# Kernel optimization log

Measured on AMD Instinct MI355X. Metric: run time of the kernel, lower is better.

The kernel has to match this reference:

```python
import jax, jax.numpy as jnp
import numpy as np

D_MODEL = 1024
D_T = 256
N_HEADS = 16
HIDDEN = 4 * D_MODEL
EPS = 1e-6


def setup_inputs() -> dict:
    key = jax.random.key(0)
    ks = jax.random.split(key, 20)
    B, L = 8, 1024
    s_d = 1.0 / np.sqrt(D_MODEL)
    s_t = 1.0 / np.sqrt(D_T)
    s_h = 1.0 / np.sqrt(HIDDEN)
    return {
        "x": jax.random.normal(ks[0], (B, L, D_MODEL), jnp.float32),
        "t": jax.random.normal(ks[1], (B, D_T), jnp.float32),
        "Wq": jax.random.normal(ks[2], (D_MODEL, D_MODEL), jnp.float32) * s_d,
        "Wk": jax.random.normal(ks[3], (D_MODEL, D_MODEL), jnp.float32) * s_d,
        "Wv": jax.random.normal(ks[4], (D_MODEL, D_MODEL), jnp.float32) * s_d,
        "Wo": jax.random.normal(ks[5], (D_MODEL, D_MODEL), jnp.float32) * s_d,
        "g1w": jax.random.normal(ks[6], (D_MODEL, D_T), jnp.float32) * s_t,
        "g1b": jnp.ones((D_MODEL,), jnp.float32),
        "b1w": jax.random.normal(ks[7], (D_MODEL, D_T), jnp.float32) * s_t,
        "b1b": jnp.zeros((D_MODEL,), jnp.float32),
        "g2w": jax.random.normal(ks[8], (D_MODEL, D_T), jnp.float32) * s_t,
        "g2b": jnp.ones((D_MODEL,), jnp.float32),
        "b2w": jax.random.normal(ks[9], (D_MODEL, D_T), jnp.float32) * s_t,
        "b2b": jnp.zeros((D_MODEL,), jnp.float32),
        "gate_w": jax.random.normal(ks[10], (HIDDEN, D_MODEL), jnp.float32) * s_d,
        "hid_w": jax.random.normal(ks[11], (HIDDEN, D_MODEL), jnp.float32) * s_d,
        "out_w": jax.random.normal(ks[12], (D_MODEL, HIDDEN), jnp.float32) * s_h,
    }


def _tc_rmsnorm(x, t, gw, gb, bw, bb):
    # gamma/beta: [B, d_model] from linear on t, broadcast over L
    g = (t @ gw.T + gb)[:, None, :]
    b = (t @ bw.T + bb)[:, None, :]
    inv_rms = jax.lax.rsqrt(jnp.mean(x * x, axis=-1, keepdims=True) + EPS)
    return g * x * inv_rms + b


def _attention(x, Wq, Wk, Wv, Wo):
    B, L, D = x.shape
    H = N_HEADS
    dh = D // H
    scale = np.sqrt(dh).astype(np.float32)
    q = (x @ Wq.T).reshape(B, L, H, dh)
    k = (x @ Wk.T).reshape(B, L, H, dh)
    v = (x @ Wv.T).reshape(B, L, H, dh)
    attn = jnp.einsum("blhd,bmhd->bhlm", q, k) / scale
    p = jax.nn.softmax(attn, axis=-1)
    o = jnp.einsum("bhlm,bmhd->blhd", p, v).reshape(B, L, D)
    return o @ Wo.T


def _swiglu(x, gate_w, hid_w, out_w):
    return (jax.nn.silu(x @ gate_w.T) * (x @ hid_w.T)) @ out_w.T


def reference(x, t, Wq, Wk, Wv, Wo, g1w, g1b, b1w, b1b, g2w, g2b, b2w, b2b, gate_w, hid_w, out_w):
    x = x + _attention(_tc_rmsnorm(x, t, g1w, g1b, b1w, b1b), Wq, Wk, Wv, Wo)
    return x + _swiglu(_tc_rmsnorm(x, t, g2w, g2b, b2w, b2b), gate_w, hid_w, out_w)
```

## Files before the change

### kernel.cpp

```cpp
#include <hip/hip_runtime.h>
#include <cstdint>
#include <cstddef>

typedef __bf16 bf16x8 __attribute__((ext_vector_type(8)));
typedef float  f32x4  __attribute__((ext_vector_type(4)));

__device__ __forceinline__ unsigned short f2bf(float f) {
  unsigned int u = __float_as_uint(f);
  u += 0x7FFFu + ((u >> 16) & 1u);
  return (unsigned short)(u >> 16);
}
__device__ __forceinline__ float bf2f(unsigned short s) {
  return __uint_as_float(((unsigned int)s) << 16);
}
__device__ __forceinline__ unsigned int pk2bf(float a, float b) {
  return (unsigned int)f2bf(a) | ((unsigned int)f2bf(b) << 16);
}

__device__ __forceinline__ void gload_lds16(const void* g, void* l) {
  __builtin_amdgcn_global_load_lds(
      (const __attribute__((address_space(1))) unsigned int*)g,
      (__attribute__((address_space(3))) unsigned int*)l, 16, 0, 0);
}

template<int EPI>
__global__ __launch_bounds__(256)
void gemm_nt(const unsigned short* __restrict__ A,
             const unsigned short* __restrict__ W,
             void* __restrict__ Cout, const void* __restrict__ aux,
             int M, int N, int K)
{
  __shared__ unsigned short As[128 * 64];
  __shared__ unsigned short Ws[128 * 64];
  const int tid  = threadIdx.x;
  const int wave = tid >> 6;
  const int lane = tid & 63;
  const int m0 = blockIdx.y << 7;
  const int n0 = blockIdx.x << 7;
  const int wm = (wave >> 1) << 6;
  const int wn = (wave & 1) << 6;

  f32x4 acc[4][4];
#pragma unroll
  for (int i = 0; i < 4; i++)
#pragma unroll
    for (int j = 0; j < 4; j++) acc[i][j] = (f32x4){0.f, 0.f, 0.f, 0.f};

  const int srow = lane >> 3;
  const int kc   = lane & 7;
  const int sc   = kc ^ srow;
  const unsigned short* pA = A + (size_t)(m0 + wave * 32 + srow) * K + sc * 8;
  const unsigned short* pW = W + (size_t)(n0 + wave * 32 + srow) * K + sc * 8;
  const size_t rstep = (size_t)8 * K;

  const int lhi = lane >> 4;
  const int l15 = lane & 15;
  const int x7  = lane & 7;
  int aoff[4], woff[4];
#pragma unroll
  for (int t = 0; t < 4; t++) {
    aoff[t] = (wm + t * 16 + l15) * 64;
    woff[t] = (wn + t * 16 + l15) * 64;
  }
  const int pos0 = (lhi ^ x7) * 8;

  for (int k0 = 0; k0 < K; k0 += 64) {
    __syncthreads();
#pragma unroll
    for (int c = 0; c < 4; c++) {
      gload_lds16(pA + (size_t)c * rstep, &As[(wave * 32 + c * 8) * 64]);
      gload_lds16(pW + (size_t)c * rstep, &Ws[(wave * 32 + c * 8) * 64]);
    }
    pA += 64; pW += 64;
    __syncthreads();
#pragma unroll
    for (int ks = 0; ks < 2; ks++) {
      const int p = pos0 ^ (ks * 32);
      bf16x8 af[4], wf[4];
#pragma unroll
      for (int t = 0; t < 4; t++) af[t] = *(const bf16x8*)&As[aoff[t] + p];
#pragma unroll
      for (int t = 0; t < 4; t++) wf[t] = *(const bf16x8*)&Ws[woff[t] + p];
#pragma unroll
      for (int i = 0; i < 4; i++)
#pragma unroll
        for (int j = 0; j < 4; j++)
          acc[i][j] = __builtin_amdgcn_mfma_f32_16x16x32_bf16(af[i], wf[j], acc[i][j], 0, 0, 0);
    }
  }

  const int erow = lhi * 4;
#pragma unroll
  for (int i = 0; i < 4; i++) {
    const int rb = m0 + wm + i * 16 + erow;
#pragma unroll
    for (int j = 0; j < 4; j++) {
      const int col = n0 + wn + j * 16 + l15;
#pragma unroll
      for (int r = 0; r < 4; r++) {
        const size_t idx = (size_t)(rb + r) * N + col;
        const float v = acc[i][j][r];
        if (EPI == 0) {
          ((unsigned short*)Cout)[idx] = f2bf(v);
        } else if (EPI == 1) {
          ((float*)Cout)[idx] = v + ((const float*)aux)[idx];
        } else {
          const float g  = bf2f(((const unsigned short*)aux)[idx]);
          const float sg = g / (1.0f + __expf(-g));
          ((unsigned short*)Cout)[idx] = f2bf(sg * v);
        }
      }
    }
  }
}

#define CEXP 0.1803368801111137f

__global__ __launch_bounds__(256, 2)
void flash_attn(const unsigned short* __restrict__ qkv,
                unsigned short* __restrict__ out)
{
  __shared__ unsigned short QP[128 * 64];
  __shared__ unsigned short Ks[64 * 64];
  __shared__ unsigned short Vt[64 * 64];
  const int tid  = threadIdx.x;
  const int wave = tid >> 6;
  const int lane = tid & 63;
  const int b  = blockIdx.x >> 4;
  const int h  = blockIdx.x & 15;
  const int qb = blockIdx.y;
  const size_t rowbase = (size_t)b * 1024 * 3072;
  const int l15 = lane & 15, lhi = lane >> 4;
  const int l7  = l15 & 7;
  const int srcb = (lane & 48) + lhi * 4;

#pragma unroll
  for (int i = 0; i < 4; i++) {
    const int ci = tid + 256 * i;
    const int r = ci >> 3, c = ci & 7;
    *(uint4*)&QP[r * 64 + c * 8] =
        *(const uint4*)&qkv[rowbase + (size_t)(qb * 128 + r) * 3072 + h * 64 + (c ^ (r & 7)) * 8];
  }
  __syncthreads();
  bf16x8 qf[2][2];
#pragma unroll
  for (int mt = 0; mt < 2; mt++)
#pragma unroll
    for (int ks = 0; ks < 2; ks++)
      qf[mt][ks] = *(const bf16x8*)&QP[(wave * 32 + mt * 16 + l15) * 64 + (((ks * 4 + lhi) ^ l7)) * 8];

  float lst[2] = {0.0f, 0.0f};
  f32x4 o[2][4];
#pragma unroll
  for (int mt = 0; mt < 2; mt++)
#pragma unroll
    for (int ct = 0; ct < 4; ct++) o[mt][ct] = (f32x4){0.f, 0.f, 0.f, 0.f};

  const int sr0 = tid >> 3;
  const int sc8 = tid & 7;
  uint4 kr[2], vr[2];
#pragma unroll
  for (int i = 0; i < 2; i++) {
    kr[i] = *(const uint4*)&qkv[rowbase + (size_t)(sr0 + 32 * i) * 3072 + 1024 + h * 64 + sc8 * 8];
    vr[i] = *(const uint4*)&qkv[rowbase + (size_t)(2 * sr0 + i) * 3072 + 2048 + h * 64 + sc8 * 8];
  }

  for (int j = 0; j < 16; j++) {
    __syncthreads();
#pragma unroll
    for (int i = 0; i < 2; i++) {
      const int r = sr0 + 32 * i;
      *(uint4*)&Ks[r * 64 + (sc8 ^ (r & 7)) * 8] = kr[i];
    }
    {
      const unsigned short* e0 = (const unsigned short*)&vr[0];
      const unsigned short* e1 = (const unsigned short*)&vr[1];
      unsigned int* VtD = (unsigned int*)Vt;
#pragma unroll
      for (int t2 = 0; t2 < 8; t2++) {
        const int d  = sc8 * 8 + t2;
        const int cs = ((sr0 >> 2) ^ t2 ^ sc8) & 7;
        VtD[d * 32 + cs * 4 + (sr0 & 3)] =
            (unsigned int)e0[t2] | ((unsigned int)e1[t2] << 16);
      }
    }
    __syncthreads();

    f32x4 s[4][2];
#pragma unroll
    for (int nt = 0; nt < 4; nt++)
#pragma unroll
      for (int mt = 0; mt < 2; mt++) s[nt][mt] = (f32x4){0.f, 0.f, 0.f, 0.f};
#pragma unroll
    for (int ks = 0; ks < 2; ks++) {
      bf16x8 kf[4];
#pragma unroll
      for (int nt = 0; nt < 4; nt++)
        kf[nt] = *(const bf16x8*)&Ks[(nt * 16 + l15) * 64 + (((ks * 4 + lhi) ^ l7)) * 8];
#pragma unroll
      for (int nt = 0; nt < 4; nt++)
#pragma unroll
        for (int mt = 0; mt < 2; mt++)
          s[nt][mt] = __builtin_amdgcn_mfma_f32_16x16x32_bf16(kf[nt], qf[mt][ks], s[nt][mt], 0, 0, 0);
    }

    {
      const int jn = ((j + 1) & 15) * 64;
#pragma unroll
      for (int i = 0; i < 2; i++) {
        kr[i] = *(const uint4*)&qkv[rowbase + (size_t)(jn + sr0 + 32 * i) * 3072 + 1024 + h * 64 + sc8 * 8];
        vr[i] = *(const uint4*)&qkv[rowbase + (size_t)(jn + 2 * sr0 + i) * 3072 + 2048 + h * 64 + sc8 * 8];
      }
    }

#pragma unroll
    for (int mt = 0; mt < 2; mt++) {
      float ls = 0.0f;
      const int prow = (wave * 32 + mt * 16 + l15) * 64;
#pragma unroll
      for (int nt = 0; nt < 4; nt++) {
        const float p0 = exp2f(s[nt][mt][0] * CEXP);
        const float p1 = exp2f(s[nt][mt][1] * CEXP);
        const float p2 = exp2f(s[nt][mt][2] * CEXP);
        const float p3 = exp2f(s[nt][mt][3] * CEXP);
        ls += (p0 + p1) + (p2 + p3);
        const int pos = ((nt * 2 + (lhi >> 1)) ^ l7);
        uint2 pk; pk.x = pk2bf(p0, p1); pk.y = pk2bf(p2, p3);
        *(uint2*)&QP[prow + pos * 8 + (lhi & 1) * 4] = pk;
      }
      lst[mt] += ls;
    }

#pragma unroll
    for (int ks = 0; ks < 2; ks++) {
      bf16x8 pf[2], vf[4];
#pragma unroll
      for (int mt = 0; mt < 2; mt++)
        pf[mt] = *(const bf16x8*)&QP[(wave * 32 + mt * 16 + l15) * 64 + (((ks * 4 + lhi) ^ l7)) * 8];
#pragma unroll
      for (int ct = 0; ct < 4; ct++) {
        const int d  = ct * 16 + l15;
        const int cs = ((ks * 4 + lhi) ^ l7 ^ (ct * 2 + (l15 >> 3))) & 7;
        vf[ct] = *(const bf16x8*)&Vt[d * 64 + cs * 8];
      }
#pragma unroll
      for (int mt = 0; mt < 2; mt++)
#pragma unroll
        for (int ct = 0; ct < 4; ct++)
          o[mt][ct] = __builtin_amdgcn_mfma_f32_16x16x32_bf16(pf[mt], vf[ct], o[mt][ct], 0, 0, 0);
    }
  }

#pragma unroll
  for (int mt = 0; mt < 2; mt++) {
    float l = lst[mt];
    l += __shfl_xor(l, 16, 64);
    l += __shfl_xor(l, 32, 64);
#pragma unroll
    for (int r = 0; r < 4; r++) {
      const float rl = 1.0f / __shfl(l, srcb + r, 64);
      const size_t row = (size_t)b * 1024 + qb * 128 + wave * 32 + mt * 16 + lhi * 4 + r;
#pragma unroll
      for (int ct = 0; ct < 4; ct++)
        out[row * 1024 + h * 64 + ct * 16 + l15] = f2bf(o[mt][ct][r] * rl);
    }
  }
}

__global__ __launch_bounds__(256)
void tc_rmsnorm_k(const float* __restrict__ x, const float* __restrict__ gamma,
                  const float* __restrict__ beta, unsigned short* __restrict__ outp)
{
  const int row = blockIdx.x;
  const int b = row >> 10;
  const int tid = threadIdx.x;
  const float4 v = *(const float4*)(x + (size_t)row * 1024 + tid * 4);
  float ss = v.x * v.x + v.y * v.y + v.z * v.z + v.w * v.w;
#pragma unroll
  for (int m = 1; m < 64; m <<= 1) ss += __shfl_xor(ss, m, 64);
  __shared__ float ws4[4];
  if ((tid & 63) == 0) ws4[tid >> 6] = ss;
  __syncthreads();
  const float inv = rsqrtf((ws4[0] + ws4[1] + ws4[2] + ws4[3]) * (1.0f / 1024.0f) + 1e-6f);
  const float4 g  = *(const float4*)(gamma + b * 1024 + tid * 4);
  const float4 be = *(const float4*)(beta  + b * 1024 + tid * 4);
  ushort4 ov;
  ov.x = f2bf(g.x * v.x * inv + be.x);
  ov.y = f2bf(g.y * v.y * inv + be.y);
  ov.z = f2bf(g.z * v.z * inv + be.z);
  ov.w = f2bf(g.w * v.w * inv + be.w);
  *(ushort4*)(outp + (size_t)row * 1024 + tid * 4) = ov;
}

__global__ __launch_bounds__(256)
void convert_bf16(const float* __restrict__ in, unsigned short* __restrict__ outp, int n)
{
  const int i = (blockIdx.x * 256 + threadIdx.x) * 4;
  if (i >= n) return;
  const float4 v = *(const float4*)(in + i);
  ushort4 ov;
  ov.x = f2bf(v.x); ov.y = f2bf(v.y); ov.z = f2bf(v.z); ov.w = f2bf(v.w);
  *(ushort4*)(outp + i) = ov;
}

__global__ __launch_bounds__(256)
void tc_linear(const float* __restrict__ t, const float* __restrict__ w,
               const float* __restrict__ bias, float* __restrict__ outp)
{
  const int idx = blockIdx.x * 256 + threadIdx.x;
  const int b = idx & 7;
  const int d = idx >> 3;
  const float* tr = t + b * 256;
  const float* wr = w + (size_t)d * 256;
  float s = bias[d];
#pragma unroll 4
  for (int k = 0; k < 256; k += 4) {
    const float4 a  = *(const float4*)(tr + k);
    const float4 ww = *(const float4*)(wr + k);
    s += a.x * ww.x + a.y * ww.y + a.z * ww.z + a.w * ww.w;
  }
  outp[b * 1024 + d] = s;
}

extern "C" void kernel_launch(void* const* d_in, const int* in_sizes, int n_in,
                              void* d_out, int out_size, void* d_ws, size_t ws_size,
                              hipStream_t stream)
{
  (void)in_sizes; (void)n_in; (void)out_size; (void)ws_size;
  const float* x     = (const float*)d_in[0];
  const float* t     = (const float*)d_in[1];
  const float* Wq    = (const float*)d_in[2];
  const float* Wk    = (const float*)d_in[3];
  const float* Wv    = (const float*)d_in[4];
  const float* Wo    = (const float*)d_in[5];
  const float* g1w   = (const float*)d_in[6];
  const float* g1b   = (const float*)d_in[7];
  const float* b1w   = (const float*)d_in[8];
  const float* b1b   = (const float*)d_in[9];
  const float* g2w   = (const float*)d_in[10];
  const float* g2b   = (const float*)d_in[11];
  const float* b2w   = (const float*)d_in[12];
  const float* b2b   = (const float*)d_in[13];
  const float* gatew = (const float*)d_in[14];
  const float* hidw  = (const float*)d_in[15];
  const float* outw  = (const float*)d_in[16];
  float* out = (float*)d_out;

  char* ws = (char*)d_ws;
  unsigned short* Wqkv_bf = (unsigned short*)(ws);
  unsigned short* Wo_bf   = (unsigned short*)(ws + 6291456);
  unsigned short* gate_bf = (unsigned short*)(ws + 8388608);
  unsigned short* hid_bf  = (unsigned short*)(ws + 16777216);
  unsigned short* outw_bf = (unsigned short*)(ws + 25165824);
  float*          gb      = (float*)(ws + 33554432);
  unsigned short* h_bf    = (unsigned short*)(ws + 33685504);
  float*          x1      = (float*)(ws + 50462720);
  unsigned short* big     = (unsigned short*)(ws + 84017152);

  convert_bf16<<<1024, 256, 0, stream>>>(Wq, Wqkv_bf,           1048576);
  convert_bf16<<<1024, 256, 0, stream>>>(Wk, Wqkv_bf + 1048576, 1048576);
  convert_bf16<<<1024, 256, 0, stream>>>(Wv, Wqkv_bf + 2097152, 1048576);
  convert_bf16<<<1024, 256, 0, stream>>>(Wo, Wo_bf,             1048576);
  convert_bf16<<<4096, 256, 0, stream>>>(gatew, gate_bf, 4194304);
  convert_bf16<<<4096, 256, 0, stream>>>(hidw,  hid_bf,  4194304);
  convert_bf16<<<4096, 256, 0, stream>>>(outw,  outw_bf, 4194304);
  tc_linear<<<32, 256, 0, stream>>>(t, g1w, g1b, gb);
  tc_linear<<<32, 256, 0, stream>>>(t, b1w, b1b, gb + 8192);
  tc_linear<<<32, 256, 0, stream>>>(t, g2w, g2b, gb + 16384);
  tc_linear<<<32, 256, 0, stream>>>(t, b2w, b2b, gb + 24576);

  tc_rmsnorm_k<<<8192, 256, 0, stream>>>(x, gb, gb + 8192, h_bf);
  gemm_nt<0><<<dim3(24, 64), 256, 0, stream>>>(h_bf, Wqkv_bf, big, nullptr, 8192, 3072, 1024);
  flash_attn<<<dim3(128, 8), 256, 0, stream>>>(big, h_bf);
  gemm_nt<1><<<dim3(8, 64), 256, 0, stream>>>(h_bf, Wo_bf, x1, x, 8192, 1024, 1024);
  tc_rmsnorm_k<<<8192, 256, 0, stream>>>(x1, gb + 16384, gb + 24576, h_bf);
  gemm_nt<0><<<dim3(32, 64), 256, 0, stream>>>(h_bf, gate_bf, big, nullptr, 8192, 4096, 1024);
  gemm_nt<2><<<dim3(32, 64), 256, 0, stream>>>(h_bf, hid_bf, big, big, 8192, 4096, 1024);
  gemm_nt<1><<<dim3(8, 64), 256, 0, stream>>>(big, outw_bf, out, x1, 8192, 1024, 4096);
}
```

Baseline: 681.6 us.

## Fuse gate and hidden SwiGLU GEMMs and add XCD-aware block swizzle

```diff
diff --git a/kernel.cpp b/kernel.cpp
--- a/kernel.cpp
+++ b/kernel.cpp
@@ -21,6 +21,15 @@
   __builtin_amdgcn_global_load_lds(
       (const __attribute__((address_space(1))) unsigned int*)g,
       (__attribute__((address_space(3))) unsigned int*)l, 16, 0, 0);
+}
+
+__device__ __forceinline__ void swizzle_xy(int& bx, int& by) {
+  const int id  = blockIdx.y * gridDim.x + blockIdx.x;
+  const int xcd = id & 7;
+  const int s   = id >> 3;
+  const int slabW = gridDim.x >> 3;
+  bx = xcd * slabW + (s >> 6);
+  by = s & 63;
 }
 
 template<int EPI>
@@ -35,8 +44,9 @@
   const int tid  = threadIdx.x;
   const int wave = tid >> 6;
   const int lane = tid & 63;
-  const int m0 = blockIdx.y << 7;
-  const int n0 = blockIdx.x << 7;
+  int bx, by; swizzle_xy(bx, by);
+  const int m0 = by << 7;
+  const int n0 = bx << 7;
   const int wm = (wave >> 1) << 6;
   const int wn = (wave & 1) << 6;
 
@@ -102,13 +112,104 @@
         const float v = acc[i][j][r];
         if (EPI == 0) {
           ((unsigned short*)Cout)[idx] = f2bf(v);
-        } else if (EPI == 1) {
+        } else {
           ((float*)Cout)[idx] = v + ((const float*)aux)[idx];
-        } else {
-          const float g  = bf2f(((const unsigned short*)aux)[idx]);
-          const float sg = g / (1.0f + __expf(-g));
-          ((unsigned short*)Cout)[idx] = f2bf(sg * v);
         }
+      }
+    }
+  }
+}
+
+__global__ __launch_bounds__(256)
+void gemm_swiglu(const unsigned short* __restrict__ A,
+                 const unsigned short* __restrict__ Wg,
+                 const unsigned short* __restrict__ Wh,
+                 unsigned short* __restrict__ Cout,
+                 int M, int N, int K)
+{
+  __shared__ unsigned short As[128 * 64];
+  __shared__ unsigned short Gs[128 * 64];
+  __shared__ unsigned short Hs[128 * 64];
+  const int tid  = threadIdx.x;
+  const int wave = tid >> 6;
+  const int lane = tid & 63;
+  int bx, by; swizzle_xy(bx, by);
+  const int m0 = by << 7;
+  const int n0 = bx << 7;
+  const int wm = (wave >> 1) << 6;
+  const int wn = (wave & 1) << 6;
+
+  f32x4 accg[4][4], acch[4][4];
+#pragma unroll
+  for (int i = 0; i < 4; i++)
+#pragma unroll
+    for (int j = 0; j < 4; j++) {
+      accg[i][j] = (f32x4){0.f, 0.f, 0.f, 0.f};
+      acch[i][j] = (f32x4){0.f, 0.f, 0.f, 0.f};
+    }
+
+  const int srow = lane >> 3;
+  const int kc   = lane & 7;
+  const int sc   = kc ^ srow;
+  const unsigned short* pA = A  + (size_t)(m0 + wave * 32 + srow) * K + sc * 8;
+  const unsigned short* pG = Wg + (size_t)(n0 + wave * 32 + srow) * K + sc * 8;
+  const unsigned short* pH = Wh + (size_t)(n0 + wave * 32 + srow) * K + sc * 8;
+  const size_t rstep = (size_t)8 * K;
+
+  const int lhi = lane >> 4;
+  const int l15 = lane & 15;
+  const int x7  = lane & 7;
+  int aoff[4], woff[4];
+#pragma unroll
+  for (int t = 0; t < 4; t++) {
+    aoff[t] = (wm + t * 16 + l15) * 64;
+    woff[t] = (wn + t * 16 + l15) * 64;
+  }
+  const int pos0 = (lhi ^ x7) * 8;
+
+  for (int k0 = 0; k0 < K; k0 += 64) {
+    __syncthreads();
+#pragma unroll
+    for (int c = 0; c < 4; c++) {
+      gload_lds16(pA + (size_t)c * rstep, &As[(wave * 32 + c * 8) * 64]);
+      gload_lds16(pG + (size_t)c * rstep, &Gs[(wave * 32 + c * 8) * 64]);
+      gload_lds16(pH + (size_t)c * rstep, &Hs[(wave * 32 + c * 8) * 64]);
+    }
+    pA += 64; pG += 64; pH += 64;
+    __syncthreads();
+#pragma unroll
+    for (int ks = 0; ks < 2; ks++) {
+      const int p = pos0 ^ (ks * 32);
+      bf16x8 af[4], gf[4], hf[4];
+#pragma unroll
+      for (int t = 0; t < 4; t++) af[t] = *(const bf16x8*)&As[aoff[t] + p];
+#pragma unroll
+      for (int t = 0; t < 4; t++) gf[t] = *(const bf16x8*)&Gs[woff[t] + p];
+#pragma unroll
+      for (int t = 0; t < 4; t++) hf[t] = *(const bf16x8*)&Hs[woff[t] + p];
+#pragma unroll
+      for (int i = 0; i < 4; i++)
+#pragma unroll
+        for (int j = 0; j < 4; j++) {
+          accg[i][j] = __builtin_amdgcn_mfma_f32_16x16x32_bf16(af[i], gf[j], accg[i][j], 0, 0, 0);
+          acch[i][j] = __builtin_amdgcn_mfma_f32_16x16x32_bf16(af[i], hf[j], acch[i][j], 0, 0, 0);
+        }
+    }
+  }
+
+  const int erow = lhi * 4;
+#pragma unroll
+  for (int i = 0; i < 4; i++) {
+    const int rb = m0 + wm + i * 16 + erow;
+#pragma unroll
+    for (int j = 0; j < 4; j++) {
+      const int col = n0 + wn + j * 16 + l15;
+#pragma unroll
+      for (int r = 0; r < 4; r++) {
+        const size_t idx = (size_t)(rb + r) * N + col;
+        const float g  = accg[i][j][r];
+        const float hv = acch[i][j][r];
+        Cout[idx] = f2bf(hv * g / (1.0f + __expf(-g)));
       }
     }
   }
@@ -374,7 +475,6 @@
   flash_attn<<<dim3(128, 8), 256, 0, stream>>>(big, h_bf);
   gemm_nt<1><<<dim3(8, 64), 256, 0, stream>>>(h_bf, Wo_bf, x1, x, 8192, 1024, 1024);
   tc_rmsnorm_k<<<8192, 256, 0, stream>>>(x1, gb + 16384, gb + 24576, h_bf);
-  gemm_nt<0><<<dim3(32, 64), 256, 0, stream>>>(h_bf, gate_bf, big, nullptr, 8192, 4096, 1024);
-  gemm_nt<2><<<dim3(32, 64), 256, 0, stream>>>(h_bf, hid_bf, big, big, 8192, 4096, 1024);
+  gemm_swiglu<<<dim3(32, 64), 256, 0, stream>>>(h_bf, gate_bf, hid_bf, big, 8192, 4096, 1024);
   gemm_nt<1><<<dim3(8, 64), 256, 0, stream>>>(big, outw_bf, out, x1, 8192, 1024, 4096);
 }
```

Result: slower. 750.3 us (+10.1%).

## Use 128x256 GEMM tiles for wide projections and merge small prep launches

Applied to the files above, without the earlier changes.

```diff
diff --git a/kernel.cpp b/kernel.cpp
--- a/kernel.cpp
+++ b/kernel.cpp
@@ -21,6 +21,89 @@
   __builtin_amdgcn_global_load_lds(
       (const __attribute__((address_space(1))) unsigned int*)g,
       (__attribute__((address_space(3))) unsigned int*)l, 16, 0, 0);
+}
+
+template<int EPI>
+__global__ __launch_bounds__(256, 2)
+void gemm_big(const unsigned short* __restrict__ A,
+              const unsigned short* __restrict__ W,
+              unsigned short* __restrict__ Cout, const unsigned short* __restrict__ aux,
+              int M, int N, int K)
+{
+  __shared__ unsigned short As[128 * 64];
+  __shared__ unsigned short Ws[256 * 64];
+  const int tid  = threadIdx.x;
+  const int wave = tid >> 6;
+  const int lane = tid & 63;
+  const int m0 = blockIdx.y << 7;
+  const int n0 = blockIdx.x << 8;
+  const int wm = (wave >> 1) << 6;
+  const int wn = (wave & 1) << 7;
+
+  f32x4 acc[4][8];
+#pragma unroll
+  for (int i = 0; i < 4; i++)
+#pragma unroll
+    for (int j = 0; j < 8; j++) acc[i][j] = (f32x4){0.f, 0.f, 0.f, 0.f};
+
+  const int srow = lane >> 3;
+  const int kc   = lane & 7;
+  const int sc   = kc ^ srow;
+  const unsigned short* pA = A + (size_t)(m0 + wave * 32 + srow) * K + sc * 8;
+  const unsigned short* pW = W + (size_t)(n0 + wave * 64 + srow) * K + sc * 8;
+  const size_t rstep = (size_t)8 * K;
+
+  const int lhi = lane >> 4;
+  const int l15 = lane & 15;
+  const int x7  = lane & 7;
+  const int pos0 = (lhi ^ x7) * 8;
+
+  for (int k0 = 0; k0 < K; k0 += 64) {
+    __syncthreads();
+#pragma unroll
+    for (int c = 0; c < 4; c++)
+      gload_lds16(pA + (size_t)c * rstep, &As[(wave * 32 + c * 8) * 64]);
+#pragma unroll
+    for (int c = 0; c < 8; c++)
+      gload_lds16(pW + (size_t)c * rstep, &Ws[(wave * 64 + c * 8) * 64]);
+    pA += 64; pW += 64;
+    __syncthreads();
+#pragma unroll
+    for (int ks = 0; ks < 2; ks++) {
+      const int p = pos0 ^ (ks * 32);
+      bf16x8 af[4];
+#pragma unroll
+      for (int t = 0; t < 4; t++) af[t] = *(const bf16x8*)&As[(wm + t * 16 + l15) * 64 + p];
+#pragma unroll
+      for (int j = 0; j < 8; j++) {
+        const bf16x8 wf = *(const bf16x8*)&Ws[(wn + j * 16 + l15) * 64 + p];
+#pragma unroll
+        for (int i = 0; i < 4; i++)
+          acc[i][j] = __builtin_amdgcn_mfma_f32_16x16x32_bf16(af[i], wf, acc[i][j], 0, 0, 0);
+      }
+    }
+  }
+
+  const int erow = lhi * 4;
+#pragma unroll
+  for (int i = 0; i < 4; i++) {
+    const int rb = m0 + wm + i * 16 + erow;
+#pragma unroll
+    for (int j = 0; j < 8; j++) {
+      const int col = n0 + wn + j * 16 + l15;
+#pragma unroll
+      for (int r = 0; r < 4; r++) {
+        const size_t idx = (size_t)(rb + r) * N + col;
+        const float v = acc[i][j][r];
+        if (EPI == 0) {
+          Cout[idx] = f2bf(v);
+        } else {
+          const float g = bf2f(aux[idx]);
+          Cout[idx] = f2bf(v * g / (1.0f + __expf(-g)));
+        }
+      }
+    }
+  }
 }
 
 template<int EPI>
@@ -102,12 +185,8 @@
         const float v = acc[i][j][r];
         if (EPI == 0) {
           ((unsigned short*)Cout)[idx] = f2bf(v);
-        } else if (EPI == 1) {
+        } else {
           ((float*)Cout)[idx] = v + ((const float*)aux)[idx];
-        } else {
-          const float g  = bf2f(((const unsigned short*)aux)[idx]);
-          const float sg = g / (1.0f + __expf(-g));
-          ((unsigned short*)Cout)[idx] = f2bf(sg * v);
         }
       }
     }
@@ -293,33 +372,50 @@
 }
 
 __global__ __launch_bounds__(256)
-void convert_bf16(const float* __restrict__ in, unsigned short* __restrict__ outp, int n)
+void convert_all(const float* __restrict__ s0, const float* __restrict__ s1,
+                 const float* __restrict__ s2, const float* __restrict__ s3,
+                 const float* __restrict__ s4, const float* __restrict__ s5,
+                 const float* __restrict__ s6, unsigned short* __restrict__ dst)
 {
   const int i = (blockIdx.x * 256 + threadIdx.x) * 4;
-  if (i >= n) return;
-  const float4 v = *(const float4*)(in + i);
+  const float* src; int off;
+  if (i < 4194304) {
+    src = (i < 1048576) ? s0 : (i < 2097152) ? s1 : (i < 3145728) ? s2 : s3;
+    off = i & 1048575;
+  } else if (i < 8388608)  { src = s4; off = i - 4194304; }
+  else if (i < 12582912)   { src = s5; off = i - 8388608; }
+  else                     { src = s6; off = i - 12582912; }
+  const float4 v = *(const float4*)(src + off);
   ushort4 ov;
   ov.x = f2bf(v.x); ov.y = f2bf(v.y); ov.z = f2bf(v.z); ov.w = f2bf(v.w);
-  *(ushort4*)(outp + i) = ov;
+  *(ushort4*)(dst + i) = ov;
 }
 
 __global__ __launch_bounds__(256)
-void tc_linear(const float* __restrict__ t, const float* __restrict__ w,
-               const float* __restrict__ bias, float* __restrict__ outp)
+void tc_linear4(const float* __restrict__ t,
+                const float* __restrict__ w0, const float* __restrict__ b0,
+                const float* __restrict__ w1, const float* __restrict__ b1,
+                const float* __restrict__ w2, const float* __restrict__ b2,
+                const float* __restrict__ w3, const float* __restrict__ b3,
+                float* __restrict__ outp)
 {
   const int idx = blockIdx.x * 256 + threadIdx.x;
-  const int b = idx & 7;
-  const int d = idx >> 3;
+  const int which = idx >> 13;
+  const int sub = idx & 8191;
+  const int b = sub & 7;
+  const int d = sub >> 3;
+  const float* w  = (which == 0) ? w0 : (which == 1) ? w1 : (which == 2) ? w2 : w3;
+  const float* bi = (which == 0) ? b0 : (which == 1) ? b1 : (which == 2) ? b2 : b3;
   const float* tr = t + b * 256;
   const float* wr = w + (size_t)d * 256;
-  float s = bias[d];
+  float s = bi[d];
 #pragma unroll 4
   for (int k = 0; k < 256; k += 4) {
     const float4 a  = *(const float4*)(tr + k);
     const float4 ww = *(const float4*)(wr + k);
     s += a.x * ww.x + a.y * ww.y + a.z * ww.z + a.w * ww.w;
   }
-  outp[b * 1024 + d] = s;
+  outp[which * 8192 + b * 1024 + d] = s;
 }
 
 extern "C" void kernel_launch(void* const* d_in, const int* in_sizes, int n_in,
@@ -357,24 +453,15 @@
   float*          x1      = (float*)(ws + 50462720);
   unsigned short* big     = (unsigned short*)(ws + 84017152);
 
-  convert_bf16<<<1024, 256, 0, stream>>>(Wq, Wqkv_bf,           1048576);
-  convert_bf16<<<1024, 256, 0, stream>>>(Wk, Wqkv_bf + 1048576, 1048576);
-  convert_bf16<<<1024, 256, 0, stream>>>(Wv, Wqkv_bf + 2097152, 1048576);
-  convert_bf16<<<1024, 256, 0, stream>>>(Wo, Wo_bf,             1048576);
-  convert_bf16<<<4096, 256, 0, stream>>>(gatew, gate_bf, 4194304);
-  convert_bf16<<<4096, 256, 0, stream>>>(hidw,  hid_bf,  4194304);
-  convert_bf16<<<4096, 256, 0, stream>>>(outw,  outw_bf, 4194304);
-  tc_linear<<<32, 256, 0, stream>>>(t, g1w, g1b, gb);
-  tc_linear<<<32, 256, 0, stream>>>(t, b1w, b1b, gb + 8192);
-  tc_linear<<<32, 256, 0, stream>>>(t, g2w, g2b, gb + 16384);
-  tc_linear<<<32, 256, 0, stream>>>(t, b2w, b2b, gb + 24576);
+  convert_all<<<16384, 256, 0, stream>>>(Wq, Wk, Wv, Wo, gatew, hidw, outw, Wqkv_bf);
+  tc_linear4<<<128, 256, 0, stream>>>(t, g1w, g1b, b1w, b1b, g2w, g2b, b2w, b2b, gb);
 
   tc_rmsnorm_k<<<8192, 256, 0, stream>>>(x, gb, gb + 8192, h_bf);
-  gemm_nt<0><<<dim3(24, 64), 256, 0, stream>>>(h_bf, Wqkv_bf, big, nullptr, 8192, 3072, 1024);
+  gemm_big<0><<<dim3(12, 64), 256, 0, stream>>>(h_bf, Wqkv_bf, big, nullptr, 8192, 3072, 1024);
   flash_attn<<<dim3(128, 8), 256, 0, stream>>>(big, h_bf);
   gemm_nt<1><<<dim3(8, 64), 256, 0, stream>>>(h_bf, Wo_bf, x1, x, 8192, 1024, 1024);
   tc_rmsnorm_k<<<8192, 256, 0, stream>>>(x1, gb + 16384, gb + 24576, h_bf);
-  gemm_nt<0><<<dim3(32, 64), 256, 0, stream>>>(h_bf, gate_bf, big, nullptr, 8192, 4096, 1024);
-  gemm_nt<2><<<dim3(32, 64), 256, 0, stream>>>(h_bf, hid_bf, big, big, 8192, 4096, 1024);
+  gemm_big<0><<<dim3(16, 64), 256, 0, stream>>>(h_bf, gate_bf, big, nullptr, 8192, 4096, 1024);
+  gemm_big<2><<<dim3(16, 64), 256, 0, stream>>>(h_bf, hid_bf, big, big, 8192, 4096, 1024);
   gemm_nt<1><<<dim3(8, 64), 256, 0, stream>>>(big, outw_bf, out, x1, 8192, 1024, 4096);
 }
```

Measured after the change: 615.5 us. -9.7%, faster.
